# Performance work log

Hardware: AMD Instinct MI355X
Metric: run time of the kernel (lower is better)

## Reference

```python
import jax, jax.numpy as jnp
import numpy as np

N_NODES = 100000
N_EDGES = 1600000
N_GRAPHS = 64
C_IN = 64
HID = 64
N_CLASSES = 10
EPS = 1e-5


def setup_inputs() -> dict:
    key = jax.random.key(0)
    ks = jax.random.split(key, 12)
    x = jax.random.normal(ks[0], (N_NODES, C_IN), dtype=jnp.float32)
    edge_index = jax.random.randint(ks[1], (2, N_EDGES), 0, N_NODES, dtype=jnp.int64)
    batch = jnp.sort(jax.random.randint(ks[2], (N_NODES,), 0, N_GRAPHS, dtype=jnp.int64))

    def lin(k, fan_in, fan_out):
        lim = 1.0 / np.sqrt(fan_in)
        kw, kb = jax.random.split(k)
        W = jax.random.uniform(kw, (fan_in, fan_out), minval=-lim, maxval=lim, dtype=jnp.float32)
        b = jax.random.uniform(kb, (fan_out,), minval=-lim, maxval=lim, dtype=jnp.float32)
        return W, b

    W1, b1 = lin(ks[3], 2 * C_IN, HID)
    W2, b2 = lin(ks[4], 2 * HID, HID)
    W3, b3 = lin(ks[5], 2 * HID, HID)
    Wo, bo = lin(ks[6], HID, N_CLASSES)
    g1 = jnp.ones((HID,), jnp.float32); be1 = jnp.zeros((HID,), jnp.float32)
    g2 = jnp.ones((HID,), jnp.float32); be2 = jnp.zeros((HID,), jnp.float32)
    g3 = jnp.ones((HID,), jnp.float32); be3 = jnp.zeros((HID,), jnp.float32)
    return {"x": x, "edge_index": edge_index, "batch": batch,
            "W1": W1, "b1": b1, "W2": W2, "b2": b2, "W3": W3, "b3": b3,
            "g1": g1, "be1": be1, "g2": g2, "be2": be2, "g3": g3, "be3": be3,
            "Wo": Wo, "bo": bo}


def edge_conv(x, src, dst, W, b):
    # PyG EdgeConv: message = mlp(cat([x_i, x_j - x_i])), aggr = max over incoming edges
    xi = x[dst]                       # target node feats [E, C]
    xj = x[src]                       # source node feats [E, C]
    m = jax.nn.relu(jnp.concatenate([xi, xj - xi], axis=-1) @ W + b)  # [E, H]
    out = jax.ops.segment_max(m, dst, num_segments=N_NODES)
    return jnp.where(jnp.isfinite(out), out, 0.0)  # nodes with no edges -> 0


def batch_norm(x, g, b):
    # training-mode BatchNorm1d over node axis, biased variance
    mu = jnp.mean(x, axis=0)
    var = jnp.mean(jnp.square(x - mu), axis=0)
    return (x - mu) * jax.lax.rsqrt(var + EPS) * g + b


def reference(x, edge_index, batch, W1, b1, W2, b2, W3, b3,
              g1, be1, g2, be2, g3, be3, Wo, bo):
    src, dst = edge_index[0], edge_index[1]
    h = edge_conv(x, src, dst, W1, b1)
    h = jax.nn.relu(batch_norm(h, g1, be1))
    h = edge_conv(h, src, dst, W2, b2)
    h = jax.nn.relu(batch_norm(h, g2, be2))
    h = edge_conv(h, src, dst, W3, b3)
    h = batch_norm(h, g3, be3)
    # global mean pool over graphs
    sums = jax.ops.segment_sum(h, batch, num_segments=N_GRAPHS)        # [G, H]
    cnts = jax.ops.segment_sum(jnp.ones((h.shape[0],), h.dtype), batch, num_segments=N_GRAPHS)
    pooled = sums / jnp.maximum(cnts, 1.0)[:, None]
    logits = pooled @ Wo + bo
    return jax.nn.softmax(logits, axis=1)
```

## Files before the change

### kernel.cpp

```cpp
#include <hip/hip_runtime.h>
#include <hip/hip_bf16.h>
#include <math.h>

#define N_NODES 100000
#define N_EDGES 1600000
#define N_GRAPHS 64
#define EPS 1e-5f
#define NBUCK 391
#define BSTRIDE 6144
#define BSCAT_GRID 196
#define SEG_NBLK 3125
#define GEMM_TILES 1563

typedef unsigned int u32;
typedef __attribute__((ext_vector_type(8))) short short8;
typedef __attribute__((ext_vector_type(4))) float f32x4;

static __device__ __forceinline__ ushort f2bf(float f) {
  u32 x = __float_as_uint(f);
  u32 r = (x + 0x7fffu + ((x >> 16) & 1u)) >> 16;
  return (ushort)r;
}
static __device__ __forceinline__ float bflo(u32 w) { return __uint_as_float(w << 16); }
static __device__ __forceinline__ float bfhi(u32 w) { return __uint_as_float(w & 0xffff0000u); }
static __device__ __forceinline__ void decode8(uint4 w, float* f) {
  f[0] = bflo(w.x); f[1] = bfhi(w.x); f[2] = bflo(w.y); f[3] = bfhi(w.y);
  f[4] = bflo(w.z); f[5] = bfhi(w.z); f[6] = bflo(w.w); f[7] = bfhi(w.w);
}

__global__ void zero_k(u32* __restrict__ p, int n) {
  int i = blockIdx.x * 256 + threadIdx.x;
  if (i < n) p[i] = 0u;
}

__global__ __launch_bounds__(256) void bscat_setup_k(
    const int* __restrict__ src, const int* __restrict__ dst,
    u32* __restrict__ bcur, u32* __restrict__ pairs,
    const float* __restrict__ W1, const float* __restrict__ W2,
    const float* __restrict__ W3, uint4* __restrict__ Wb,
    const int* __restrict__ batch, u32* __restrict__ bounds,
    u32* __restrict__ zbase) {
  __shared__ u32 cnt[NBUCK];
  __shared__ u32 base[NBUCK];
  int bid = blockIdx.x, t = threadIdx.x;
  if (bid < BSCAT_GRID) {
    for (int i = t; i < NBUCK; i += 256) cnt[i] = 0;
    __syncthreads();
    u32 pk[32], bk[32];
    int be = bid * 8192;
#pragma unroll
    for (int k = 0; k < 32; ++k) {
      int e = be + k * 256 + t;
      if (e < N_EDGES) {
        u32 d = (u32)dst[e], s = (u32)src[e];
        u32 b = d >> 8;
        pk[k] = ((d & 255u) << 24) | s;
        bk[k] = b;
        atomicAdd(&cnt[b], 1u);
      } else bk[k] = 0xFFFFFFFFu;
    }
    __syncthreads();
    for (int i = t; i < NBUCK; i += 256) {
      u32 c = cnt[i];
      base[i] = c ? (i * BSTRIDE + atomicAdd(&bcur[i], c)) : 0u;
      cnt[i] = 0;
    }
    __syncthreads();
#pragma unroll
    for (int k = 0; k < 32; ++k) {
      if (bk[k] != 0xFFFFFFFFu) {
        u32 p = base[bk[k]] + atomicAdd(&cnt[bk[k]], 1u);
        pairs[p] = pk[k];
      }
    }
  } else if (bid < BSCAT_GRID + 12) {
    int g = (bid - BSCAT_GRID) * 256 + t;
    if (g >= 3072) return;
    int layer = g >> 10, rem = g & 1023;
    int kh = rem >> 9, ct = (rem >> 6) & 7, l = rem & 63;
    const float* W = (layer == 0) ? W1 : (layer == 1) ? W2 : W3;
    int c = ct * 16 + (l & 15);
    u32 w[4];
#pragma unroll
    for (int jj = 0; jj < 4; ++jj) {
      int k0 = kh * 32 + (l >> 4) * 8 + 2 * jj;
      float v0, v1;
      if (c < 64) {
        v0 = W[k0 * 64 + c] - W[(64 + k0) * 64 + c];
        v1 = W[(k0 + 1) * 64 + c] - W[(65 + k0) * 64 + c];
      } else {
        v0 = W[(64 + k0) * 64 + (c - 64)];
        v1 = W[(65 + k0) * 64 + (c - 64)];
      }
      w[jj] = (u32)f2bf(v0) | ((u32)f2bf(v1) << 16);
    }
    Wb[g] = make_uint4(w[0], w[1], w[2], w[3]);
  } else if (bid == BSCAT_GRID + 12) {
    if (t > 64) return;
    int lo = 0, hi = N_NODES;
    while (lo < hi) {
      int mid = (lo + hi) >> 1;
      if (batch[mid] < t) lo = mid + 1; else hi = mid;
    }
    bounds[t] = (u32)lo;
  } else {
    for (int i = t; i < 16384; i += 256) zbase[i] = 0u;
  }
}

static __device__ __forceinline__ void fscat2_body(
    int b, u32* SH, const u32* __restrict__ bcur, const u32* __restrict__ pairs,
    u32* __restrict__ esrc, u32* __restrict__ offs_g, u32* __restrict__ cnt_g) {
  u32* lcnt = SH; u32* lexc = SH + 256; u32* lcur = SH + 512;
  int t = threadIdx.x;
  u32 s0 = b * BSTRIDE, e0 = s0 + bcur[b];
  lcnt[t] = 0;
  __syncthreads();
  for (u32 p = s0 + t; p < e0; p += 256) atomicAdd(&lcnt[pairs[p] >> 24], 1u);
  __syncthreads();
  u32 v = lcnt[t];
  lexc[t] = v;
  __syncthreads();
  for (int d = 1; d < 256; d <<= 1) {
    u32 a = (t >= d) ? lexc[t - d] : 0u;
    __syncthreads();
    lexc[t] += a;
    __syncthreads();
  }
  u32 excl = lexc[t] - v;
  int node = (b << 8) + t;
  if (node < N_NODES) { offs_g[node] = s0 + excl; cnt_g[node] = v; }
  lcur[t] = 0;
  lexc[t] = excl;
  __syncthreads();
  for (u32 p = s0 + t; p < e0; p += 256) {
    u32 pk = pairs[p];
    u32 dl = pk >> 24;
    u32 l = atomicAdd(&lcur[dl], 1u);
    esrc[s0 + lexc[dl] + l] = pk & 0x00FFFFFFu;
  }
}

static __device__ __forceinline__ void gemm_body(
    int tile, u32* Xl,
    const void* __restrict__ xin, int xbf16, const uint4* __restrict__ Wb,
    const float* ab, const float* __restrict__ bias,
    ushort* __restrict__ ub, ushort* __restrict__ vb) {
  int t = threadIdx.x;
  int l = t & 63, wv = t >> 6;
  short8 bs[2][8];
#pragma unroll
  for (int kh = 0; kh < 2; ++kh)
#pragma unroll
    for (int ct = 0; ct < 8; ++ct) {
      uint4 tmp = Wb[(kh * 8 + ct) * 64 + l];
      __builtin_memcpy(&bs[kh][ct], &tmp, 16);
    }
  int srow = t >> 2, scol = (t & 3) * 16;
  int rb = tile * 64;
  int gr = rb + srow;
  u32 xb[8];
  if (gr < N_NODES) {
    if (xbf16) {
      const uint4* xp = (const uint4*)((const ushort*)xin + (size_t)gr * 64 + scol);
      uint4 p0 = xp[0], p1 = xp[1];
      u32 raw[8] = {p0.x, p0.y, p0.z, p0.w, p1.x, p1.y, p1.z, p1.w};
#pragma unroll
      for (int q = 0; q < 8; ++q) {
        int c = scol + 2 * q;
        float lo = fmaxf(fmaf(bflo(raw[q]), ab[c], ab[64 + c]), 0.f);
        float hi = fmaxf(fmaf(bfhi(raw[q]), ab[c + 1], ab[64 + c + 1]), 0.f);
        xb[q] = (u32)f2bf(lo) | ((u32)f2bf(hi) << 16);
      }
    } else {
      const float4* xp = (const float4*)((const float*)xin + (size_t)gr * 64 + scol);
#pragma unroll
      for (int q = 0; q < 4; ++q) {
        float4 a = xp[q];
        xb[2 * q]     = (u32)f2bf(a.x) | ((u32)f2bf(a.y) << 16);
        xb[2 * q + 1] = (u32)f2bf(a.z) | ((u32)f2bf(a.w) << 16);
      }
    }
  } else {
#pragma unroll
    for (int q = 0; q < 8; ++q) xb[q] = 0u;
  }
  int byte0 = srow * 128 + ((scol * 2) ^ ((srow & 7) << 4));
  int byte1 = srow * 128 + ((scol * 2 + 16) ^ ((srow & 7) << 4));
  *(uint4*)((char*)Xl + byte0) = make_uint4(xb[0], xb[1], xb[2], xb[3]);
  *(uint4*)((char*)Xl + byte1) = make_uint4(xb[4], xb[5], xb[6], xb[7]);
  __syncthreads();
  f32x4 acc[8];
#pragma unroll
  for (int ct = 0; ct < 8; ++ct) {
    float b0 = (ct < 4) ? bias[ct * 16 + (l & 15)] : 0.f;
    acc[ct] = (f32x4){b0, b0, b0, b0};
  }
  int arow = wv * 16 + (l & 15);
#pragma unroll
  for (int kh = 0; kh < 2; ++kh) {
    int abyte = arow * 128 + ((kh * 64 + ((l >> 4) * 16)) ^ ((arow & 7) << 4));
    short8 af = *(const short8*)((const char*)Xl + abyte);
#pragma unroll
    for (int ct = 0; ct < 8; ++ct)
      acc[ct] = __builtin_amdgcn_mfma_f32_16x16x32_bf16(af, bs[kh][ct], acc[ct], 0, 0, 0);
  }
  int rloc = rb + wv * 16 + 4 * (l >> 4);
#pragma unroll
  for (int ct = 0; ct < 4; ++ct) {
    int col = ct * 16 + (l & 15);
#pragma unroll
    for (int r = 0; r < 4; ++r) {
      int row = rloc + r;
      if (row < N_NODES) ub[(size_t)row * 64 + col] = f2bf(acc[ct][r]);
    }
  }
#pragma unroll
  for (int ct = 4; ct < 8; ++ct) {
    int col = ct * 16 + (l & 15) - 64;
#pragma unroll
    for (int r = 0; r < 4; ++r) {
      int row = rloc + r;
      if (row < N_NODES) vb[(size_t)row * 64 + col] = f2bf(acc[ct][r]);
    }
  }
}

__global__ __launch_bounds__(256) void fused_fg_k(
    const u32* __restrict__ bcur, const u32* __restrict__ pairs,
    u32* __restrict__ esrc, u32* __restrict__ offs_g, u32* __restrict__ cnt_g,
    const float* __restrict__ x, const uint4* __restrict__ Wb,
    const float* __restrict__ bias, ushort* __restrict__ ub, ushort* __restrict__ vb) {
  __shared__ u32 SH[2048];
  int bid = blockIdx.x;
  if (bid < NBUCK) fscat2_body(bid, SH, bcur, pairs, esrc, offs_g, cnt_g);
  else gemm_body(bid - NBUCK, SH, x, 0, Wb, nullptr, bias, ub, vb);
}

__global__ __launch_bounds__(256) void gemm_k(
    const ushort* __restrict__ xin, const uint4* __restrict__ Wb,
    const float* __restrict__ bnacc, const float* __restrict__ g,
    const float* __restrict__ be, const float* __restrict__ bias,
    ushort* __restrict__ ub, ushort* __restrict__ vb) {
  __shared__ u32 Xl[2048];
  __shared__ float ab_sh[128];
  int t = threadIdx.x;
  if (t < 64) {
    float s1 = 0.f, s2 = 0.f;
    for (int s = 0; s < 32; ++s) {
      s1 += bnacc[s * 128 + t];
      s2 += bnacc[s * 128 + 64 + t];
    }
    float mu = s1 / (float)N_NODES;
    float var = s2 / (float)N_NODES - mu * mu;
    float al = g[t] / sqrtf(var + EPS);
    ab_sh[t] = al;
    ab_sh[64 + t] = be[t] - mu * al;
  }
  __syncthreads();
  gemm_body(blockIdx.x, Xl, xin, 1, Wb, ab_sh, bias, ub, vb);
}

template <int LAST>
__global__ __launch_bounds__(256) void segmax_k(
    const ushort* __restrict__ v, const u32* __restrict__ offs,
    const u32* __restrict__ cnt, const u32* __restrict__ esrc,
    const ushort* __restrict__ ub, ushort* __restrict__ hb,
    float* __restrict__ bnacc, const u32* __restrict__ bounds,
    float* __restrict__ sums) {
  __shared__ float red[2048];
  __shared__ u32 bsh[65];
  __shared__ int gmin_sh, mflag;
  int t = threadIdx.x;
  if (LAST) {
    if (t < 65) bsh[t] = bounds[t];
    if (t == 0) mflag = 0;
    __syncthreads();
  }
  int lane = t & 63;
  int op = lane & 7;
  int sub = lane >> 3;
  int wv = t >> 6;
  int node = blockIdx.x * 32 + wv * 8 + sub;
  const uint4* v4 = (const uint4*)v;
  const uint4* u4 = (const uint4*)ub;
  u32 off = offs[node], deg = cnt[node];
  const u32* ep = esrc + off;
  float m[8];
#pragma unroll
  for (int j = 0; j < 8; ++j) m[j] = -INFINITY;
  u32 i = 0;
  for (; i + 4 <= deg; i += 4) {
    u32 sA = ep[i], sB = ep[i + 1], sC = ep[i + 2], sD = ep[i + 3];
    uint4 wA = v4[(size_t)sA * 8 + op];
    uint4 wB = v4[(size_t)sB * 8 + op];
    uint4 wC = v4[(size_t)sC * 8 + op];
    uint4 wD = v4[(size_t)sD * 8 + op];
    float fA[8], fB[8], fC[8], fD[8];
    decode8(wA, fA); decode8(wB, fB); decode8(wC, fC); decode8(wD, fD);
#pragma unroll
    for (int j = 0; j < 8; ++j)
      m[j] = fmaxf(fmaxf(m[j], fmaxf(fA[j], fB[j])), fmaxf(fC[j], fD[j]));
  }
  for (; i < deg; ++i) {
    uint4 w = v4[(size_t)ep[i] * 8 + op];
    float f[8]; decode8(w, f);
#pragma unroll
    for (int j = 0; j < 8; ++j) m[j] = fmaxf(m[j], f[j]);
  }
  uint4 uu = u4[(size_t)node * 8 + op];
  float uf[8]; decode8(uu, uf);
  float h[8];
#pragma unroll
  for (int j = 0; j < 8; ++j) h[j] = fmaxf(uf[j] + m[j], 0.f);
  int g = 0;
  if (LAST) {
    int lo = 0, hi = N_GRAPHS - 1;
    while (lo < hi) {
      int mid = (lo + hi + 1) >> 1;
      if (bsh[mid] <= (u32)node) lo = mid; else hi = mid - 1;
    }
    g = lo;
    if (t == 0) gmin_sh = g;
  } else {
    uint4 hw;
    hw.x = (u32)f2bf(h[0]) | ((u32)f2bf(h[1]) << 16);
    hw.y = (u32)f2bf(h[2]) | ((u32)f2bf(h[3]) << 16);
    hw.z = (u32)f2bf(h[4]) | ((u32)f2bf(h[5]) << 16);
    hw.w = (u32)f2bf(h[6]) | ((u32)f2bf(h[7]) << 16);
    ((uint4*)hb)[(size_t)node * 8 + op] = hw;
  }
#pragma unroll
  for (int j = 0; j < 8; ++j) red[t * 8 + j] = h[j];
  __syncthreads();
  float o1 = 0.f, o2 = 0.f;
  int cop = t >> 3, cj = t & 7;
  if (t < 64) {
    for (int q = 0; q < 32; ++q) o1 += red[(q * 8 + cop) * 8 + cj];
  }
  __syncthreads();
#pragma unroll
  for (int j = 0; j < 8; ++j) red[t * 8 + j] = h[j] * h[j];
  __syncthreads();
  if (t < 64) {
    for (int q = 0; q < 32; ++q) o2 += red[(q * 8 + cop) * 8 + cj];
    int slice = blockIdx.x & 31;
    atomicAdd(&bnacc[slice * 128 + t], o1);
    atomicAdd(&bnacc[slice * 128 + 64 + t], o2);
  }
  if (LAST) {
    __syncthreads();
    int gmin = gmin_sh;
    int slot = g - gmin;
#pragma unroll
    for (int j = 0; j < 8; ++j) red[t * 8 + j] = (slot == 0) ? h[j] : 0.f;
    if (slot != 0) mflag = 1;
    __syncthreads();
    if (t < 64) {
      float o = 0.f;
      for (int q = 0; q < 32; ++q) o += red[(q * 8 + cop) * 8 + cj];
      atomicAdd(&sums[gmin * 64 + t], o);
    }
    if (mflag) {
      __syncthreads();
#pragma unroll
      for (int j = 0; j < 8; ++j) red[t * 8 + j] = (slot == 1) ? h[j] : 0.f;
      __syncthreads();
      if (t < 64) {
        float o = 0.f;
        for (int q = 0; q < 32; ++q) o += red[(q * 8 + cop) * 8 + cj];
        atomicAdd(&sums[(gmin + 1) * 64 + t], o);
      }
      if (slot >= 2) {
#pragma unroll
        for (int j = 0; j < 8; ++j) atomicAdd(&sums[g * 64 + op * 8 + j], h[j]);
      }
    }
  }
}

__global__ void head_k(const float* __restrict__ sums, const u32* __restrict__ bounds,
                       const float* __restrict__ bnacc3, const float* __restrict__ g3,
                       const float* __restrict__ be3, const float* __restrict__ Wo,
                       const float* __restrict__ bo, float* __restrict__ out) {
  __shared__ float ab3[128];
  int t = threadIdx.x;
  if (t < 64) {
    float s1 = 0.f, s2 = 0.f;
    for (int sl = 0; sl < 32; ++sl) {
      s1 += bnacc3[sl * 128 + t];
      s2 += bnacc3[sl * 128 + 64 + t];
    }
    float mu = s1 / (float)N_NODES;
    float var = s2 / (float)N_NODES - mu * mu;
    float al = g3[t] / sqrtf(var + EPS);
    ab3[t] = al;
    ab3[64 + t] = be3[t] - mu * al;
  }
  __syncthreads();
  if (t >= N_GRAPHS) return;
  u32 cntn = bounds[t + 1] - bounds[t];
  float inv = (cntn > 0) ? 1.f / (float)cntn : 0.f;
  float lg[10];
#pragma unroll
  for (int j = 0; j < 10; ++j) lg[j] = bo[j];
  for (int c = 0; c < 64; ++c) {
    float p = (cntn > 0) ? (sums[t * 64 + c] * inv * ab3[c] + ab3[64 + c]) : 0.f;
#pragma unroll
    for (int j = 0; j < 10; ++j) lg[j] = fmaf(p, Wo[c * 10 + j], lg[j]);
  }
  float mx = lg[0];
#pragma unroll
  for (int j = 1; j < 10; ++j) mx = fmaxf(mx, lg[j]);
  float ssum = 0.f, ex[10];
#pragma unroll
  for (int j = 0; j < 10; ++j) { ex[j] = expf(lg[j] - mx); ssum += ex[j]; }
#pragma unroll
  for (int j = 0; j < 10; ++j) out[t * 10 + j] = ex[j] / ssum;
}

extern "C" void kernel_launch(void* const* d_in, const int* in_sizes, int n_in,
                              void* d_out, int out_size, void* d_ws, size_t ws_size,
                              hipStream_t stream) {
  const float* x    = (const float*)d_in[0];
  const int*   ei   = (const int*)d_in[1];
  const int*   batch= (const int*)d_in[2];
  const float* W1 = (const float*)d_in[3];  const float* b1 = (const float*)d_in[4];
  const float* W2 = (const float*)d_in[5];  const float* b2 = (const float*)d_in[6];
  const float* W3 = (const float*)d_in[7];  const float* b3 = (const float*)d_in[8];
  const float* g1 = (const float*)d_in[9];  const float* be1= (const float*)d_in[10];
  const float* g2 = (const float*)d_in[11]; const float* be2= (const float*)d_in[12];
  const float* g3 = (const float*)d_in[13]; const float* be3= (const float*)d_in[14];
  const float* Wo = (const float*)d_in[15]; const float* bo = (const float*)d_in[16];
  float* out = (float*)d_out;

  char* p = (char*)d_ws;
  auto alloc = [&](size_t bytes) { void* r = (void*)p; p += (bytes + 255) & ~(size_t)255; return r; };
  uint4* Wb     = (uint4*)alloc(3072 * sizeof(uint4));
  u32*   bounds = (u32*)alloc(65 * sizeof(u32));
  u32*   bcur   = (u32*)alloc(NBUCK * sizeof(u32));
  u32*   cnt    = (u32*)alloc((size_t)N_NODES * sizeof(u32));
  u32*   offs   = (u32*)alloc((size_t)N_NODES * sizeof(u32));
  float* sums   = (float*)alloc(4096 * sizeof(float));
  float* bnacc  = (float*)alloc(12288 * sizeof(float));
  u32*   esrc   = (u32*)alloc((size_t)NBUCK * BSTRIDE * sizeof(u32));
  u32*   pairs  = (u32*)alloc((size_t)NBUCK * BSTRIDE * sizeof(u32));
  ushort* ub    = (ushort*)alloc((size_t)N_NODES * 64 * sizeof(ushort));
  ushort* vb    = (ushort*)alloc((size_t)N_NODES * 64 * sizeof(ushort));
  ushort* hb    = (ushort*)alloc((size_t)N_NODES * 64 * sizeof(ushort));

  const int* src = ei;
  const int* dst = ei + N_EDGES;

  zero_k<<<2, 256, 0, stream>>>(bcur, NBUCK);
  bscat_setup_k<<<BSCAT_GRID + 14, 256, 0, stream>>>(src, dst, bcur, pairs,
                                                     W1, W2, W3, Wb, batch, bounds,
                                                     (u32*)sums);

  fused_fg_k<<<NBUCK + GEMM_TILES, 256, 0, stream>>>(bcur, pairs, esrc, offs, cnt,
                                                     x, Wb, b1, ub, vb);
  segmax_k<0><<<SEG_NBLK, 256, 0, stream>>>(vb, offs, cnt, esrc, ub, hb, bnacc,
                                            bounds, sums);

  gemm_k<<<GEMM_TILES, 256, 0, stream>>>(hb, Wb + 1024, bnacc, g1, be1, b2, ub, vb);
  segmax_k<0><<<SEG_NBLK, 256, 0, stream>>>(vb, offs, cnt, esrc, ub, hb, bnacc + 4096,
                                            bounds, sums);

  gemm_k<<<GEMM_TILES, 256, 0, stream>>>(hb, Wb + 2048, bnacc + 4096, g2, be2, b3, ub, vb);
  segmax_k<1><<<SEG_NBLK, 256, 0, stream>>>(vb, offs, cnt, esrc, ub, hb, bnacc + 8192,
                                            bounds, sums);

  head_k<<<1, 64, 0, stream>>>(sums, bounds, bnacc + 8192, g3, be3, Wo, bo, out);
}
```

Measured before the change: 202.9 us.

## Process two GEMM tiles per block, halve bucket-scatter chunk, unroll segmax by 8

GEMM blocks now each handle two 64-row tiles and load the weight fragments into registers once, reusing them across both tiles. This halves the GEMM launch count and the redundant weight loads. The bucket scatter setup doubles its grid and halves edges per block for more parallelism. The segment-max gather loop now unrolls 8 edges at a time to keep more loads in flight, at the cost of more registers and a possible occupancy drop.

```diff
diff --git a/kernel.cpp b/kernel.cpp
--- a/kernel.cpp
+++ b/kernel.cpp
@@ -8,9 +8,10 @@
 #define EPS 1e-5f
 #define NBUCK 391
 #define BSTRIDE 6144
-#define BSCAT_GRID 196
+#define BSCAT_GRID 391
 #define SEG_NBLK 3125
 #define GEMM_TILES 1563
+#define GEMM_BLOCKS 782
 
 typedef unsigned int u32;
 typedef __attribute__((ext_vector_type(8))) short short8;
@@ -46,10 +47,10 @@
   if (bid < BSCAT_GRID) {
     for (int i = t; i < NBUCK; i += 256) cnt[i] = 0;
     __syncthreads();
-    u32 pk[32], bk[32];
-    int be = bid * 8192;
-#pragma unroll
-    for (int k = 0; k < 32; ++k) {
+    u32 pk[16], bk[16];
+    int be = bid * 4096;
+#pragma unroll
+    for (int k = 0; k < 16; ++k) {
       int e = be + k * 256 + t;
       if (e < N_EDGES) {
         u32 d = (u32)dst[e], s = (u32)src[e];
@@ -67,7 +68,7 @@
     }
     __syncthreads();
 #pragma unroll
-    for (int k = 0; k < 32; ++k) {
+    for (int k = 0; k < 16; ++k) {
       if (bk[k] != 0xFFFFFFFFu) {
         u32 p = base[bk[k]] + atomicAdd(&cnt[bk[k]], 1u);
         pairs[p] = pk[k];
@@ -141,21 +142,26 @@
   }
 }
 
-static __device__ __forceinline__ void gemm_body(
-    int tile, u32* Xl,
-    const void* __restrict__ xin, int xbf16, const uint4* __restrict__ Wb,
+struct WFrags { short8 bs[2][8]; };
+
+static __device__ __forceinline__ void load_wfrags(const uint4* __restrict__ Wb,
+                                                   int l, WFrags& wf) {
+#pragma unroll
+  for (int kh = 0; kh < 2; ++kh)
+#pragma unroll
+    for (int ct = 0; ct < 8; ++ct) {
+      uint4 tmp = Wb[(kh * 8 + ct) * 64 + l];
+      __builtin_memcpy(&wf.bs[kh][ct], &tmp, 16);
+    }
+}
+
+static __device__ __forceinline__ void gemm_tile(
+    int tile, u32* Xl, const WFrags& wf,
+    const void* __restrict__ xin, int xbf16,
     const float* ab, const float* __restrict__ bias,
     ushort* __restrict__ ub, ushort* __restrict__ vb) {
   int t = threadIdx.x;
   int l = t & 63, wv = t >> 6;
-  short8 bs[2][8];
-#pragma unroll
-  for (int kh = 0; kh < 2; ++kh)
-#pragma unroll
-    for (int ct = 0; ct < 8; ++ct) {
-      uint4 tmp = Wb[(kh * 8 + ct) * 64 + l];
-      __builtin_memcpy(&bs[kh][ct], &tmp, 16);
-    }
   int srow = t >> 2, scol = (t & 3) * 16;
   int rb = tile * 64;
   int gr = rb + srow;
@@ -203,7 +209,7 @@
     short8 af = *(const short8*)((const char*)Xl + abyte);
 #pragma unroll
     for (int ct = 0; ct < 8; ++ct)
-      acc[ct] = __builtin_amdgcn_mfma_f32_16x16x32_bf16(af, bs[kh][ct], acc[ct], 0, 0, 0);
+      acc[ct] = __builtin_amdgcn_mfma_f32_16x16x32_bf16(af, wf.bs[kh][ct], acc[ct], 0, 0, 0);
   }
   int rloc = rb + wv * 16 + 4 * (l >> 4);
 #pragma unroll
@@ -223,6 +229,22 @@
       int row = rloc + r;
       if (row < N_NODES) vb[(size_t)row * 64 + col] = f2bf(acc[ct][r]);
     }
+  }
+}
+
+static __device__ __forceinline__ void gemm_2tiles(
+    int tile0, u32* Xl, const uint4* __restrict__ Wb,
+    const void* __restrict__ xin, int xbf16,
+    const float* ab, const float* __restrict__ bias,
+    ushort* __restrict__ ub, ushort* __restrict__ vb) {
+  WFrags wf;
+  load_wfrags(Wb, threadIdx.x & 63, wf);
+#pragma unroll
+  for (int tt = 0; tt < 2; ++tt) {
+    int tile = tile0 + tt;
+    if (tile >= GEMM_TILES) break;
+    if (tt) __syncthreads();
+    gemm_tile(tile, Xl, wf, xin, xbf16, ab, bias, ub, vb);
   }
 }
 
@@ -234,7 +256,7 @@
   __shared__ u32 SH[2048];
   int bid = blockIdx.x;
   if (bid < NBUCK) fscat2_body(bid, SH, bcur, pairs, esrc, offs_g, cnt_g);
-  else gemm_body(bid - NBUCK, SH, x, 0, Wb, nullptr, bias, ub, vb);
+  else gemm_2tiles((bid - NBUCK) * 2, SH, Wb, x, 0, nullptr, bias, ub, vb);
 }
 
 __global__ __launch_bounds__(256) void gemm_k(
@@ -258,7 +280,7 @@
     ab_sh[64 + t] = be[t] - mu * al;
   }
   __syncthreads();
-  gemm_body(blockIdx.x, Xl, xin, 1, Wb, ab_sh, bias, ub, vb);
+  gemm_2tiles(blockIdx.x * 2, Xl, Wb, xin, 1, ab_sh, bias, ub, vb);
 }
 
 template <int LAST>
@@ -290,17 +312,38 @@
 #pragma unroll
   for (int j = 0; j < 8; ++j) m[j] = -INFINITY;
   u32 i = 0;
+  for (; i + 8 <= deg; i += 8) {
+    u32 s0 = ep[i], s1 = ep[i+1], s2 = ep[i+2], s3 = ep[i+3];
+    u32 s4 = ep[i+4], s5 = ep[i+5], s6 = ep[i+6], s7 = ep[i+7];
+    uint4 w0 = v4[(size_t)s0 * 8 + op];
+    uint4 w1 = v4[(size_t)s1 * 8 + op];
+    uint4 w2 = v4[(size_t)s2 * 8 + op];
+    uint4 w3 = v4[(size_t)s3 * 8 + op];
+    uint4 w4 = v4[(size_t)s4 * 8 + op];
+    uint4 w5 = v4[(size_t)s5 * 8 + op];
+    uint4 w6 = v4[(size_t)s6 * 8 + op];
+    uint4 w7 = v4[(size_t)s7 * 8 + op];
+    float f0[8], f1[8], f2[8], f3[8], f4[8], f5[8], f6[8], f7[8];
+    decode8(w0, f0); decode8(w1, f1); decode8(w2, f2); decode8(w3, f3);
+    decode8(w4, f4); decode8(w5, f5); decode8(w6, f6); decode8(w7, f7);
+#pragma unroll
+    for (int j = 0; j < 8; ++j) {
+      float a = fmaxf(fmaxf(f0[j], f1[j]), fmaxf(f2[j], f3[j]));
+      float b = fmaxf(fmaxf(f4[j], f5[j]), fmaxf(f6[j], f7[j]));
+      m[j] = fmaxf(m[j], fmaxf(a, b));
+    }
+  }
   for (; i + 4 <= deg; i += 4) {
-    u32 sA = ep[i], sB = ep[i + 1], sC = ep[i + 2], sD = ep[i + 3];
-    uint4 wA = v4[(size_t)sA * 8 + op];
-    uint4 wB = v4[(size_t)sB * 8 + op];
-    uint4 wC = v4[(size_t)sC * 8 + op];
-    uint4 wD = v4[(size_t)sD * 8 + op];
-    float fA[8], fB[8], fC[8], fD[8];
-    decode8(wA, fA); decode8(wB, fB); decode8(wC, fC); decode8(wD, fD);
+    u32 s0 = ep[i], s1 = ep[i+1], s2 = ep[i+2], s3 = ep[i+3];
+    uint4 w0 = v4[(size_t)s0 * 8 + op];
+    uint4 w1 = v4[(size_t)s1 * 8 + op];
+    uint4 w2 = v4[(size_t)s2 * 8 + op];
+    uint4 w3 = v4[(size_t)s3 * 8 + op];
+    float f0[8], f1[8], f2[8], f3[8];
+    decode8(w0, f0); decode8(w1, f1); decode8(w2, f2); decode8(w3, f3);
 #pragma unroll
     for (int j = 0; j < 8; ++j)
-      m[j] = fmaxf(fmaxf(m[j], fmaxf(fA[j], fB[j])), fmaxf(fC[j], fD[j]));
+      m[j] = fmaxf(m[j], fmaxf(fmaxf(f0[j], f1[j]), fmaxf(f2[j], f3[j])));
   }
   for (; i < deg; ++i) {
     uint4 w = v4[(size_t)ep[i] * 8 + op];
@@ -457,16 +500,16 @@
                                                      W1, W2, W3, Wb, batch, bounds,
                                                      (u32*)sums);
 
-  fused_fg_k<<<NBUCK + GEMM_TILES, 256, 0, stream>>>(bcur, pairs, esrc, offs, cnt,
-                                                     x, Wb, b1, ub, vb);
+  fused_fg_k<<<NBUCK + GEMM_BLOCKS, 256, 0, stream>>>(bcur, pairs, esrc, offs, cnt,
+                                                      x, Wb, b1, ub, vb);
   segmax_k<0><<<SEG_NBLK, 256, 0, stream>>>(vb, offs, cnt, esrc, ub, hb, bnacc,
                                             bounds, sums);
 
-  gemm_k<<<GEMM_TILES, 256, 0, stream>>>(hb, Wb + 1024, bnacc, g1, be1, b2, ub, vb);
+  gemm_k<<<GEMM_BLOCKS, 256, 0, stream>>>(hb, Wb + 1024, bnacc, g1, be1, b2, ub, vb);
   segmax_k<0><<<SEG_NBLK, 256, 0, stream>>>(vb, offs, cnt, esrc, ub, hb, bnacc + 4096,
                                             bounds, sums);
 
-  gemm_k<<<GEMM_TILES, 256, 0, stream>>>(hb, Wb + 2048, bnacc + 4096, g2, be2, b3, ub, vb);
+  gemm_k<<<GEMM_BLOCKS, 256, 0, stream>>>(hb, Wb + 2048, bnacc + 4096, g2, be2, b3, ub, vb);
   segmax_k<1><<<SEG_NBLK, 256, 0, stream>>>(vb, offs, cnt, esrc, ub, hb, bnacc + 8192,
                                             bounds, sums);
 
```

Result: no change. 205.9 us (+1.5%).
